# Kernel tuning notes

Hardware: AMD Instinct MI355X
Metric: run time of the kernel (lower is better)

## Reference

```python
import jax, jax.numpy as jnp
import numpy as np

K = 2  # top-k slots from init kwargs


def setup_inputs() -> dict:
    key = jax.random.key(0)
    ks = jax.random.split(key, 6)
    B, T, d, E, dff = 2, 2048, 512, 8, 2048
    x = jax.random.normal(ks[0], (B, T, d), dtype=jnp.float32)
    Wg = jax.random.normal(ks[1], (d, E), dtype=jnp.float32) * 0.02
    W1 = jax.random.normal(ks[2], (E, d, dff), dtype=jnp.float32) * 0.02
    b1 = jnp.zeros((E, dff), dtype=jnp.float32)
    W2 = jax.random.normal(ks[3], (E, dff, d), dtype=jnp.float32) * 0.02
    b2 = jnp.zeros((E, d), dtype=jnp.float32)
    return {"x": x, "Wg": Wg, "W1": W1, "b1": b1, "W2": W2, "b2": b2}


def reference(x, Wg, W1, b1, W2, b2):
    # Gate: softmax over experts, top-k probs renormalized. Note: in the
    # original code the per-expert gather/scatter masks partition the tokens,
    # so dispatched_input == x * p_i (full weighted input), and ALL experts'
    # MLPs are applied to it and summed (tf.add_n). We reproduce that math.
    logits = jnp.einsum('btd,de->bte', x, Wg)          # [B,T,E]
    probs = jax.nn.softmax(logits, axis=-1)
    top_p, _top_i = jax.lax.top_k(probs, K)            # [B,T,K]
    top_p = top_p / jnp.sum(top_p, axis=-1, keepdims=True)
    b2_sum = jnp.sum(b2, axis=0)                        # sum of all experts' output biases
    out = jnp.zeros_like(x)
    for i in range(K):  # small fixed loop over top-k slots
        w_in = x * top_p[..., i:i + 1]                  # [B,T,d]
        # every expert runs on the full weighted input (faithful to source)
        h = jax.nn.gelu(
            jnp.einsum('btd,edf->ebtf', w_in, W1) + b1[:, None, None, :],
            approximate=False)                           # [E,B,T,dff]
        out = out + jnp.einsum('ebtf,efd->btd', h, W2) + b2_sum
    return out
```

## Files before the change

kernel.cpp:

```cpp
#include <hip/hip_runtime.h>
#include <hip/hip_bf16.h>
#include <cstdint>

#define TOKENS 4096
#define DMODEL 512
#define NEXP 8
#define DFF 2048

typedef short s16x8 __attribute__((ext_vector_type(8)));
typedef short s16x4 __attribute__((ext_vector_type(4)));
typedef float f32x4 __attribute__((ext_vector_type(4)));

__device__ __forceinline__ float bf2f(short h) {
    unsigned int u = ((unsigned int)(unsigned short)h) << 16;
    return __uint_as_float(u);
}
__device__ __forceinline__ short f2bf(float f) {
    unsigned int u = __float_as_uint(f);
    u += 0x7fffu + ((u >> 16) & 1u);
    return (short)(u >> 16);
}
__device__ __forceinline__ float gelu_f(float x) {
    float x2 = x * x;
    float z2 = x * fmaf(x2, 0.07135481627260025f, 1.5957691216057308f);
    float ex = __expf(z2);
    float r = __builtin_amdgcn_rcpf(1.0f + ex);
    return x - x * r;
}
__device__ __forceinline__ void gload_lds16(const void* g, void* l) {
    __builtin_amdgcn_global_load_lds((const __attribute__((address_space(1))) void*)g,
                                     (__attribute__((address_space(3))) void*)l, 16, 0, 0);
}

__global__ void gate_cvt_kernel(const float* __restrict__ x, const float* __restrict__ Wg,
                                float* __restrict__ s0, float* __restrict__ s1,
                                short* __restrict__ xb) {
    int wave = threadIdx.x >> 6;
    int lane = threadIdx.x & 63;
    int t = blockIdx.x * 4 + wave;
    const float* xr = x + (size_t)t * DMODEL + lane * 8;
    float4 xa = *(const float4*)(xr);
    float4 xv2 = *(const float4*)(xr + 4);
    float xv[8] = {xa.x, xa.y, xa.z, xa.w, xv2.x, xv2.y, xv2.z, xv2.w};
    s16x8 v;
#pragma unroll
    for (int j = 0; j < 8; j++) v[j] = f2bf(xv[j]);
    *(s16x8*)&xb[(size_t)t * DMODEL + lane * 8] = v;

    float lg[8];
#pragma unroll
    for (int e = 0; e < 8; e++) lg[e] = 0.f;
#pragma unroll
    for (int j = 0; j < 8; j++) {
        const float4* wr = (const float4*)(Wg + (size_t)(lane * 8 + j) * NEXP);
        float4 wa = wr[0], wb = wr[1];
        lg[0] = fmaf(xv[j], wa.x, lg[0]);
        lg[1] = fmaf(xv[j], wa.y, lg[1]);
        lg[2] = fmaf(xv[j], wa.z, lg[2]);
        lg[3] = fmaf(xv[j], wa.w, lg[3]);
        lg[4] = fmaf(xv[j], wb.x, lg[4]);
        lg[5] = fmaf(xv[j], wb.y, lg[5]);
        lg[6] = fmaf(xv[j], wb.z, lg[6]);
        lg[7] = fmaf(xv[j], wb.w, lg[7]);
    }
#pragma unroll
    for (int off = 32; off > 0; off >>= 1) {
#pragma unroll
        for (int e = 0; e < 8; e++) lg[e] += __shfl_xor(lg[e], off, 64);
    }
    float l0 = lg[0]; int i0 = 0;
#pragma unroll
    for (int e = 1; e < 8; e++) { if (lg[e] > l0) { l0 = lg[e]; i0 = e; } }
    float l1 = -3.4e38f;
#pragma unroll
    for (int e = 0; e < 8; e++) { if (e != i0 && lg[e] > l1) l1 = lg[e]; }
    float p1 = expf(l1 - l0);
    float sa = 1.0f / (1.0f + p1);
    if (lane == 0) { s0[t] = sa; s1[t] = p1 * sa; }
}

__global__ void transpose_cvt_kernel(const float* __restrict__ in, short* __restrict__ out,
                                     int R, int C) {
    __shared__ float t[64][33];
    int b = blockIdx.z;
    const float* ip = in + (size_t)b * R * C;
    short* op = out + (size_t)b * R * C;
    int c0 = blockIdx.x * 64, r0 = blockIdx.y * 32;
    int tid = threadIdx.x;
    int lr = tid >> 3, lc8 = (tid & 7) * 8;
    const float* src = &ip[(size_t)(r0 + lr) * C + c0 + lc8];
    float4 v0 = *(const float4*)src;
    float4 v1 = *(const float4*)(src + 4);
    t[lc8 + 0][lr] = v0.x; t[lc8 + 1][lr] = v0.y; t[lc8 + 2][lr] = v0.z; t[lc8 + 3][lr] = v0.w;
    t[lc8 + 4][lr] = v1.x; t[lc8 + 5][lr] = v1.y; t[lc8 + 6][lr] = v1.z; t[lc8 + 7][lr] = v1.w;
    __syncthreads();
    int sc = tid >> 2, sk = (tid & 3) * 8;
    s16x8 o;
#pragma unroll
    for (int j = 0; j < 8; j++) o[j] = f2bf(t[sc][sk + j]);
    *(s16x8*)&op[(size_t)(c0 + sc) * R + r0 + sk] = o;
}

__launch_bounds__(256, 2)
__global__ void gemm1_kernel(const short* __restrict__ xb, const short* __restrict__ w1t,
                             const float* __restrict__ s0v, const float* __restrict__ s1v,
                             const float* __restrict__ b1, short* __restrict__ H) {
    __shared__ short Al[128 * 64];
    __shared__ short Bl[128 * 64];
    __shared__ float ls0[128], ls1[128], lb1[128];
    int d = blockIdx.x;
    int e = d & 7;
    int tno = d >> 3;
    int n0 = (tno & 15) * 128;
    int m0 = (tno >> 4) * 128;
    const short* A = xb;
    const short* B = w1t + (size_t)e * DFF * DMODEL;
    short* Ho = H + (size_t)e * TOKENS * DFF;

    int tid = threadIdx.x;
    int lane = tid & 63;
    int w = tid >> 6;
    int m_off = (w >> 1) * 64;
    int n_off = (w & 1) * 64;

    if (tid < 128) {
        ls0[tid] = s0v[m0 + tid];
        ls1[tid] = s1v[m0 + tid];
        lb1[tid] = b1[(size_t)e * DFF + n0 + tid];
    }

    int srow = lane >> 3;
    int schunk = (lane & 7) ^ srow;
    int q = lane >> 4;

    f32x4 acc[4][4];
#pragma unroll
    for (int mi = 0; mi < 4; mi++)
#pragma unroll
        for (int ni = 0; ni < 4; ni++) acc[mi][ni] = (f32x4){0.f, 0.f, 0.f, 0.f};

    for (int k0 = 0; k0 < DMODEL; k0 += 64) {
#pragma unroll
        for (int c = 0; c < 4; c++) {
            int seg = c * 4 + w;
            gload_lds16(&A[(size_t)(m0 + seg * 8 + srow) * DMODEL + k0 + schunk * 8],
                        &Al[seg * 512]);
            gload_lds16(&B[(size_t)(n0 + seg * 8 + srow) * DMODEL + k0 + schunk * 8],
                        &Bl[seg * 512]);
        }
        __syncthreads();
#pragma unroll
        for (int ks = 0; ks < 2; ks++) {
            s16x8 af[4], bfr[4];
#pragma unroll
            for (int mi = 0; mi < 4; mi++) {
                int r = m_off + mi * 16 + (lane & 15);
                int cp = (ks * 4 + q) ^ (r & 7);
                af[mi] = *(const s16x8*)&Al[r * 64 + cp * 8];
            }
#pragma unroll
            for (int ni = 0; ni < 4; ni++) {
                int r = n_off + ni * 16 + (lane & 15);
                int cp = (ks * 4 + q) ^ (r & 7);
                bfr[ni] = *(const s16x8*)&Bl[r * 64 + cp * 8];
            }
#pragma unroll
            for (int mi = 0; mi < 4; mi++)
#pragma unroll
                for (int ni = 0; ni < 4; ni++)
                    acc[mi][ni] = __builtin_amdgcn_mfma_f32_16x16x32_bf16(af[mi], bfr[ni], acc[mi][ni], 0, 0, 0);
        }
        __syncthreads();
    }
#pragma unroll
    for (int mi = 0; mi < 4; mi++) {
        int rl = m_off + mi * 16 + (lane >> 4) * 4;
        float sa4[4], sb4[4];
#pragma unroll
        for (int r = 0; r < 4; r++) { sa4[r] = ls0[rl + r]; sb4[r] = ls1[rl + r]; }
#pragma unroll
        for (int ni = 0; ni < 4; ni++) {
            int cl = n_off + ni * 16 + (lane & 15);
            float bb = lb1[cl];
#pragma unroll
            for (int r = 0; r < 4; r++) {
                float a = acc[mi][ni][r];
                float h = gelu_f(fmaf(sa4[r], a, bb)) + gelu_f(fmaf(sb4[r], a, bb));
                Ho[(size_t)(m0 + rl + r) * DFF + n0 + cl] = f2bf(h);
            }
        }
    }
}

__launch_bounds__(256, 2)
__global__ void gemm2_kernel(const short* __restrict__ H, const short* __restrict__ w2t,
                             float* __restrict__ part) {
    __shared__ short Al[128 * 64];
    __shared__ short Bl[128 * 64];
    int d = blockIdx.x;
    int e = d & 7;
    int tno = d >> 3;
    int n0 = (tno & 3) * 128;
    int m0 = (tno >> 2) * 128;
    const short* A = H + (size_t)e * TOKENS * DFF;
    const short* B = w2t + (size_t)e * DMODEL * DFF;
    float* Pe = part + (size_t)e * TOKENS * DMODEL;

    int tid = threadIdx.x;
    int lane = tid & 63;
    int w = tid >> 6;
    int m_off = (w >> 1) * 64;
    int n_off = (w & 1) * 64;

    int srow = lane >> 3;
    int schunk = (lane & 7) ^ srow;
    int q = lane >> 4;

    f32x4 acc[4][4];
#pragma unroll
    for (int mi = 0; mi < 4; mi++)
#pragma unroll
        for (int ni = 0; ni < 4; ni++) acc[mi][ni] = (f32x4){0.f, 0.f, 0.f, 0.f};

    for (int k0 = 0; k0 < DFF; k0 += 64) {
#pragma unroll
        for (int c = 0; c < 4; c++) {
            int seg = c * 4 + w;
            gload_lds16(&A[(size_t)(m0 + seg * 8 + srow) * DFF + k0 + schunk * 8],
                        &Al[seg * 512]);
            gload_lds16(&B[(size_t)(n0 + seg * 8 + srow) * DFF + k0 + schunk * 8],
                        &Bl[seg * 512]);
        }
        __syncthreads();
#pragma unroll
        for (int ks = 0; ks < 2; ks++) {
            s16x8 af[4], bfr[4];
#pragma unroll
            for (int mi = 0; mi < 4; mi++) {
                int r = m_off + mi * 16 + (lane & 15);
                int cp = (ks * 4 + q) ^ (r & 7);
                af[mi] = *(const s16x8*)&Al[r * 64 + cp * 8];
            }
#pragma unroll
            for (int ni = 0; ni < 4; ni++) {
                int r = n_off + ni * 16 + (lane & 15);
                int cp = (ks * 4 + q) ^ (r & 7);
                bfr[ni] = *(const s16x8*)&Bl[r * 64 + cp * 8];
            }
#pragma unroll
            for (int mi = 0; mi < 4; mi++)
#pragma unroll
                for (int ni = 0; ni < 4; ni++)
                    acc[mi][ni] = __builtin_amdgcn_mfma_f32_16x16x32_bf16(af[mi], bfr[ni], acc[mi][ni], 0, 0, 0);
        }
        __syncthreads();
    }

#pragma unroll
    for (int mi = 0; mi < 4; mi++)
#pragma unroll
        for (int ni = 0; ni < 4; ni++) {
            int row = m0 + m_off + mi * 16 + (lane >> 4) * 4;
            int col = n0 + n_off + ni * 16 + (lane & 15);
#pragma unroll
            for (int r = 0; r < 4; r++)
                Pe[(size_t)(row + r) * DMODEL + col] = acc[mi][ni][r];
        }
}

__global__ void reduce_kernel(const float* __restrict__ part, const float* __restrict__ b2,
                              float* __restrict__ out) {
    int i = (blockIdx.x * 256 + threadIdx.x) * 4;
    if (i >= TOKENS * DMODEL) return;
    int n = i & (DMODEL - 1);
    float4 s = {0.f, 0.f, 0.f, 0.f};
    float4 bs = {0.f, 0.f, 0.f, 0.f};
#pragma unroll
    for (int e = 0; e < 8; e++) {
        float4 p = *(const float4*)&part[(size_t)e * TOKENS * DMODEL + i];
        s.x += p.x; s.y += p.y; s.z += p.z; s.w += p.w;
        float4 b = *(const float4*)&b2[(size_t)e * DMODEL + n];
        bs.x += b.x; bs.y += b.y; bs.z += b.z; bs.w += b.w;
    }
    s.x += 2.f * bs.x; s.y += 2.f * bs.y; s.z += 2.f * bs.z; s.w += 2.f * bs.w;
    *(float4*)&out[i] = s;
}

extern "C" void kernel_launch(void* const* d_in, const int* in_sizes, int n_in,
                              void* d_out, int out_size, void* d_ws, size_t ws_size,
                              hipStream_t stream) {
    const float* x  = (const float*)d_in[0];
    const float* Wg = (const float*)d_in[1];
    const float* W1 = (const float*)d_in[2];
    const float* b1 = (const float*)d_in[3];
    const float* W2 = (const float*)d_in[4];
    const float* b2 = (const float*)d_in[5];
    float* out = (float*)d_out;

    char* ws = (char*)d_ws;
    float* s0  = (float*)(ws);
    float* s1  = (float*)(ws + 16384);
    short* xb  = (short*)(ws + 32768);
    short* w1t = (short*)(ws + 32768 + 4194304);
    short* w2t = (short*)(ws + 32768 + 4194304 + 16777216);
    short* Hb  = (short*)(ws + 32768 + 4194304 + 2ull * 16777216);
    float* part= (float*)(ws + 32768 + 4194304 + 2ull * 16777216 + 134217728);

    hipLaunchKernelGGL(gate_cvt_kernel, dim3(1024), dim3(256), 0, stream, x, Wg, s0, s1, xb);
    hipLaunchKernelGGL(transpose_cvt_kernel, dim3(32, 16, 8), dim3(256), 0, stream, W1, w1t, 512, 2048);
    hipLaunchKernelGGL(transpose_cvt_kernel, dim3(8, 64, 8), dim3(256), 0, stream, W2, w2t, 2048, 512);
    hipLaunchKernelGGL(gemm1_kernel, dim3(4096), dim3(256), 0, stream, xb, w1t, s0, s1, b1, Hb);
    hipLaunchKernelGGL(gemm2_kernel, dim3(1024), dim3(256), 0, stream, Hb, w2t, part);
    hipLaunchKernelGGL(reduce_kernel, dim3(2048), dim3(256), 0, stream, part, b2, out);
}
```

Before: 210.4 us.

## Triple-buffer gemm2 with 256x128 tiles and 512-thread blocks

Reworks the second expert GEMM so each 512-thread block computes a 256x128 output tile. Global-to-LDS loads go through a three-stage ring buffer with explicit vmcnt waits and raw barriers, so loads for later K-slices overlap MFMA compute on the current one. The larger tile halves the grid and improves reuse of the W2 tile. In exchange LDS use grows to about 144 KB per block, occupancy drops to one block per CU, and correctness depends on hand-tuned wait counts.

```diff
diff --git a/kernel.cpp b/kernel.cpp
--- a/kernel.cpp
+++ b/kernel.cpp
@@ -192,18 +192,56 @@
     }
 }
 
-__launch_bounds__(256, 2)
+__device__ __forceinline__ void g2_stage(const short* __restrict__ A, const short* __restrict__ B,
+                                         short* Al, short* Bl, int k0, int w, int srow, int schunk) {
+#pragma unroll
+    for (int c = 0; c < 4; c++) {
+        int seg = c * 8 + w;
+        gload_lds16(&A[(size_t)(seg * 8 + srow) * DFF + k0 + schunk * 8], &Al[seg * 512]);
+    }
+#pragma unroll
+    for (int c = 0; c < 2; c++) {
+        int seg = c * 8 + w;
+        gload_lds16(&B[(size_t)(seg * 8 + srow) * DFF + k0 + schunk * 8], &Bl[seg * 512]);
+    }
+}
+__device__ __forceinline__ void g2_compute(const short* Al, const short* Bl, f32x4 acc[4][4],
+                                           int m_off, int n_off, int lane, int q) {
+#pragma unroll
+    for (int ks = 0; ks < 2; ks++) {
+        s16x8 af[4], bfr[4];
+#pragma unroll
+        for (int mi = 0; mi < 4; mi++) {
+            int r = m_off + mi * 16 + (lane & 15);
+            int cp = (ks * 4 + q) ^ (r & 7);
+            af[mi] = *(const s16x8*)&Al[r * 64 + cp * 8];
+        }
+#pragma unroll
+        for (int ni = 0; ni < 4; ni++) {
+            int r = n_off + ni * 16 + (lane & 15);
+            int cp = (ks * 4 + q) ^ (r & 7);
+            bfr[ni] = *(const s16x8*)&Bl[r * 64 + cp * 8];
+        }
+#pragma unroll
+        for (int mi = 0; mi < 4; mi++)
+#pragma unroll
+            for (int ni = 0; ni < 4; ni++)
+                acc[mi][ni] = __builtin_amdgcn_mfma_f32_16x16x32_bf16(af[mi], bfr[ni], acc[mi][ni], 0, 0, 0);
+    }
+}
+
+__launch_bounds__(512, 1)
 __global__ void gemm2_kernel(const short* __restrict__ H, const short* __restrict__ w2t,
                              float* __restrict__ part) {
-    __shared__ short Al[128 * 64];
-    __shared__ short Bl[128 * 64];
+    __shared__ short Al[3][256 * 64];
+    __shared__ short Bl[3][128 * 64];
     int d = blockIdx.x;
     int e = d & 7;
     int tno = d >> 3;
     int n0 = (tno & 3) * 128;
-    int m0 = (tno >> 2) * 128;
-    const short* A = H + (size_t)e * TOKENS * DFF;
-    const short* B = w2t + (size_t)e * DMODEL * DFF;
+    int m0 = (tno >> 2) * 256;
+    const short* A = H + (size_t)e * TOKENS * DFF + (size_t)m0 * DFF;
+    const short* B = w2t + (size_t)e * DMODEL * DFF + (size_t)n0 * DFF;
     float* Pe = part + (size_t)e * TOKENS * DMODEL;
 
     int tid = threadIdx.x;
@@ -211,10 +249,10 @@
     int w = tid >> 6;
     int m_off = (w >> 1) * 64;
     int n_off = (w & 1) * 64;
+    int q = lane >> 4;
 
     int srow = lane >> 3;
     int schunk = (lane & 7) ^ srow;
-    int q = lane >> 4;
 
     f32x4 acc[4][4];
 #pragma unroll
@@ -222,38 +260,33 @@
 #pragma unroll
         for (int ni = 0; ni < 4; ni++) acc[mi][ni] = (f32x4){0.f, 0.f, 0.f, 0.f};
 
-    for (int k0 = 0; k0 < DFF; k0 += 64) {
-#pragma unroll
-        for (int c = 0; c < 4; c++) {
-            int seg = c * 4 + w;
-            gload_lds16(&A[(size_t)(m0 + seg * 8 + srow) * DFF + k0 + schunk * 8],
-                        &Al[seg * 512]);
-            gload_lds16(&B[(size_t)(n0 + seg * 8 + srow) * DFF + k0 + schunk * 8],
-                        &Bl[seg * 512]);
-        }
-        __syncthreads();
-#pragma unroll
-        for (int ks = 0; ks < 2; ks++) {
-            s16x8 af[4], bfr[4];
-#pragma unroll
-            for (int mi = 0; mi < 4; mi++) {
-                int r = m_off + mi * 16 + (lane & 15);
-                int cp = (ks * 4 + q) ^ (r & 7);
-                af[mi] = *(const s16x8*)&Al[r * 64 + cp * 8];
-            }
-#pragma unroll
-            for (int ni = 0; ni < 4; ni++) {
-                int r = n_off + ni * 16 + (lane & 15);
-                int cp = (ks * 4 + q) ^ (r & 7);
-                bfr[ni] = *(const s16x8*)&Bl[r * 64 + cp * 8];
-            }
-#pragma unroll
-            for (int mi = 0; mi < 4; mi++)
-#pragma unroll
-                for (int ni = 0; ni < 4; ni++)
-                    acc[mi][ni] = __builtin_amdgcn_mfma_f32_16x16x32_bf16(af[mi], bfr[ni], acc[mi][ni], 0, 0, 0);
-        }
-        __syncthreads();
+    const int NT = DFF / 64;
+
+    g2_stage(A, B, Al[0], Bl[0], 0, w, srow, schunk);
+    g2_stage(A, B, Al[1], Bl[1], 64, w, srow, schunk);
+
+    for (int t = 0; t < NT - 2; t++) {
+        g2_stage(A, B, Al[(t + 2) % 3], Bl[(t + 2) % 3], (t + 2) * 64, w, srow, schunk);
+        asm volatile("s_waitcnt vmcnt(12)" ::: "memory");
+        __builtin_amdgcn_s_barrier();
+        __builtin_amdgcn_sched_barrier(0);
+        g2_compute(Al[t % 3], Bl[t % 3], acc, m_off, n_off, lane, q);
+        __builtin_amdgcn_sched_barrier(0);
+        __builtin_amdgcn_s_barrier();
+    }
+    {
+        asm volatile("s_waitcnt vmcnt(6)" ::: "memory");
+        __builtin_amdgcn_s_barrier();
+        __builtin_amdgcn_sched_barrier(0);
+        g2_compute(Al[(NT - 2) % 3], Bl[(NT - 2) % 3], acc, m_off, n_off, lane, q);
+        __builtin_amdgcn_sched_barrier(0);
+        __builtin_amdgcn_s_barrier();
+    }
+    {
+        asm volatile("s_waitcnt vmcnt(0)" ::: "memory");
+        __builtin_amdgcn_s_barrier();
+        __builtin_amdgcn_sched_barrier(0);
+        g2_compute(Al[(NT - 1) % 3], Bl[(NT - 1) % 3], acc, m_off, n_off, lane, q);
     }
 
 #pragma unroll
@@ -310,6 +343,6 @@
     hipLaunchKernelGGL(transpose_cvt_kernel, dim3(32, 16, 8), dim3(256), 0, stream, W1, w1t, 512, 2048);
     hipLaunchKernelGGL(transpose_cvt_kernel, dim3(8, 64, 8), dim3(256), 0, stream, W2, w2t, 2048, 512);
     hipLaunchKernelGGL(gemm1_kernel, dim3(4096), dim3(256), 0, stream, xb, w1t, s0, s1, b1, Hb);
-    hipLaunchKernelGGL(gemm2_kernel, dim3(1024), dim3(256), 0, stream, Hb, w2t, part);
+    hipLaunchKernelGGL(gemm2_kernel, dim3(512), dim3(512), 0, stream, Hb, w2t, part);
     hipLaunchKernelGGL(reduce_kernel, dim3(2048), dim3(256), 0, stream, part, b2, out);
 }
```

Result: slower. 233.2 us (+10.9%).

## Transpose MFMA operands for vectorized epilogue stores and fuse paired GELU evaluation

Applied to the files above, without the earlier changes.

Swaps the A/B operands of the MFMA calls so each lane holds four consecutive output columns of one row. The epilogues can then write packed bf16x4 (gemm1) and float4 (gemm2) stores instead of scalar ones. GELU of the two top-k slots is merged into one function that uses exp2 and a single shared reciprocal, and bf16 packing uses the hardware v_cvt_pk_bf16_f32 instruction. This is meant to cut store instruction count and transcendental work in the epilogue. The exp2-based rewrite slightly changes rounding, and the shared reciprocal of a product could overflow for large inputs.

```diff
diff --git a/kernel.cpp b/kernel.cpp
--- a/kernel.cpp
+++ b/kernel.cpp
@@ -10,6 +10,7 @@
 typedef short s16x8 __attribute__((ext_vector_type(8)));
 typedef short s16x4 __attribute__((ext_vector_type(4)));
 typedef float f32x4 __attribute__((ext_vector_type(4)));
+typedef unsigned int u32x2 __attribute__((ext_vector_type(2)));
 
 __device__ __forceinline__ float bf2f(short h) {
     unsigned int u = ((unsigned int)(unsigned short)h) << 16;
@@ -19,6 +20,11 @@
     unsigned int u = __float_as_uint(f);
     u += 0x7fffu + ((u >> 16) & 1u);
     return (short)(u >> 16);
+}
+__device__ __forceinline__ unsigned int cvtpk_bf16(float a, float b) {
+    unsigned int r;
+    asm volatile("v_cvt_pk_bf16_f32 %0, %1, %2" : "=v"(r) : "v"(a), "v"(b));
+    return r;
 }
 __device__ __forceinline__ float gelu_f(float x) {
     float x2 = x * x;
@@ -26,6 +32,18 @@
     float ex = __expf(z2);
     float r = __builtin_amdgcn_rcpf(1.0f + ex);
     return x - x * r;
+}
+#define GP_C0 2.3022084f
+#define GP_C1 0.10294330f
+__device__ __forceinline__ float gelu_pair(float x0, float x1) {
+    float z0 = x0 * fmaf(x0 * x0, GP_C1, GP_C0);
+    float z1 = x1 * fmaf(x1 * x1, GP_C1, GP_C0);
+    float e0 = __builtin_amdgcn_exp2f(z0);
+    float e1 = __builtin_amdgcn_exp2f(z1);
+    float t0 = 1.0f + e0, t1 = 1.0f + e1;
+    float R = __builtin_amdgcn_rcpf(t0 * t1);
+    float num = fmaf(x0, t1, x1 * t0);
+    return fmaf(-num, R, x0 + x1);
 }
 __device__ __forceinline__ void gload_lds16(const void* g, void* l) {
     __builtin_amdgcn_global_load_lds((const __attribute__((address_space(1))) void*)g,
@@ -168,25 +186,32 @@
             for (int mi = 0; mi < 4; mi++)
 #pragma unroll
                 for (int ni = 0; ni < 4; ni++)
-                    acc[mi][ni] = __builtin_amdgcn_mfma_f32_16x16x32_bf16(af[mi], bfr[ni], acc[mi][ni], 0, 0, 0);
+                    acc[mi][ni] = __builtin_amdgcn_mfma_f32_16x16x32_bf16(bfr[ni], af[mi], acc[mi][ni], 0, 0, 0);
         }
         __syncthreads();
     }
-#pragma unroll
-    for (int mi = 0; mi < 4; mi++) {
-        int rl = m_off + mi * 16 + (lane >> 4) * 4;
-        float sa4[4], sb4[4];
-#pragma unroll
-        for (int r = 0; r < 4; r++) { sa4[r] = ls0[rl + r]; sb4[r] = ls1[rl + r]; }
-#pragma unroll
-        for (int ni = 0; ni < 4; ni++) {
-            int cl = n_off + ni * 16 + (lane & 15);
-            float bb = lb1[cl];
-#pragma unroll
-            for (int r = 0; r < 4; r++) {
-                float a = acc[mi][ni][r];
-                float h = gelu_f(fmaf(sa4[r], a, bb)) + gelu_f(fmaf(sb4[r], a, bb));
-                Ho[(size_t)(m0 + rl + r) * DFF + n0 + cl] = f2bf(h);
+    {
+        int mcol = lane & 15;
+        int nrow4 = (lane >> 4) * 4;
+#pragma unroll
+        for (int mi = 0; mi < 4; mi++) {
+            int m = m_off + mi * 16 + mcol;
+            float sa = ls0[m], sb = ls1[m];
+#pragma unroll
+            for (int ni = 0; ni < 4; ni++) {
+                int nb = n_off + ni * 16 + nrow4;
+                float4 bb = *(const float4*)&lb1[nb];
+                float bv[4] = {bb.x, bb.y, bb.z, bb.w};
+                float h4[4];
+#pragma unroll
+                for (int r = 0; r < 4; r++) {
+                    float a = acc[mi][ni][r];
+                    h4[r] = gelu_pair(fmaf(sa, a, bv[r]), fmaf(sb, a, bv[r]));
+                }
+                u32x2 pv;
+                pv[0] = cvtpk_bf16(h4[0], h4[1]);
+                pv[1] = cvtpk_bf16(h4[2], h4[3]);
+                *(u32x2*)&Ho[(size_t)(m0 + m) * DFF + n0 + nb] = pv;
             }
         }
     }
@@ -251,21 +276,24 @@
             for (int mi = 0; mi < 4; mi++)
 #pragma unroll
                 for (int ni = 0; ni < 4; ni++)
-                    acc[mi][ni] = __builtin_amdgcn_mfma_f32_16x16x32_bf16(af[mi], bfr[ni], acc[mi][ni], 0, 0, 0);
+                    acc[mi][ni] = __builtin_amdgcn_mfma_f32_16x16x32_bf16(bfr[ni], af[mi], acc[mi][ni], 0, 0, 0);
         }
         __syncthreads();
     }
 
-#pragma unroll
-    for (int mi = 0; mi < 4; mi++)
-#pragma unroll
-        for (int ni = 0; ni < 4; ni++) {
-            int row = m0 + m_off + mi * 16 + (lane >> 4) * 4;
-            int col = n0 + n_off + ni * 16 + (lane & 15);
-#pragma unroll
-            for (int r = 0; r < 4; r++)
-                Pe[(size_t)(row + r) * DMODEL + col] = acc[mi][ni][r];
-        }
+    {
+        int mcol = lane & 15;
+        int nrow4 = (lane >> 4) * 4;
+#pragma unroll
+        for (int mi = 0; mi < 4; mi++) {
+            int m = m0 + m_off + mi * 16 + mcol;
+#pragma unroll
+            for (int ni = 0; ni < 4; ni++) {
+                int nb = n0 + n_off + ni * 16 + nrow4;
+                *(f32x4*)&Pe[(size_t)m * DMODEL + nb] = acc[mi][ni];
+            }
+        }
+    }
 }
 
 __global__ void reduce_kernel(const float* __restrict__ part, const float* __restrict__ b2,
```

After: 215.1 us. +2.3%, slower.
